# Optimization experiments

Measured on AMD Instinct MI355X. Metric: run time of the kernel, lower is better.

Reference implementation:

```python
import jax, jax.numpy as jnp
import numpy as np

B, S, D = 4, 2048, 1024
H, DK, DV = 16, 64, 64
FF = 4096
EPS = 1e-6


def _ln(x, g, b):
    mu = jnp.mean(x, axis=-1, keepdims=True)
    var = jnp.mean((x - mu) ** 2, axis=-1, keepdims=True)
    return (x - mu) * jax.lax.rsqrt(var + EPS) * g + b


def setup_inputs() -> dict:
    key = jax.random.key(0)
    ks = jax.random.split(key, 12)
    sd = 0.02
    return {
        "src": jax.random.normal(ks[0], (B, S, D), jnp.float32),
        "attn_mask": jnp.zeros((B, S, S), jnp.bool_),
        "Wq": jax.random.normal(ks[1], (D, H * DK), jnp.float32) * sd,
        "bq": jnp.zeros((H * DK,), jnp.float32),
        "Wk": jax.random.normal(ks[2], (D, H * DK), jnp.float32) * sd,
        "bk": jnp.zeros((H * DK,), jnp.float32),
        "Wv": jax.random.normal(ks[3], (D, H * DV), jnp.float32) * sd,
        "bv": jnp.zeros((H * DV,), jnp.float32),
        "Wo": jax.random.normal(ks[4], (D, D), jnp.float32) * sd,
        "bo": jnp.zeros((D,), jnp.float32),
        "ln1_g": jnp.ones((D,), jnp.float32),
        "ln1_b": jnp.zeros((D,), jnp.float32),
        "W1": jax.random.normal(ks[5], (D, FF), jnp.float32) * sd,
        "b1": jnp.zeros((FF,), jnp.float32),
        "W2": jax.random.normal(ks[6], (FF, D), jnp.float32) * sd,
        "b2": jnp.zeros((D,), jnp.float32),
        "ln2_g": jnp.ones((D,), jnp.float32),
        "ln2_b": jnp.zeros((D,), jnp.float32),
    }


def reference(src, attn_mask, Wq, bq, Wk, bk, Wv, bv, Wo, bo,
              ln1_g, ln1_b, W1, b1, W2, b2, ln2_g, ln2_b):
    # QKV projections, split heads: [B,S,H*dk] -> [B,H,S,dk]
    q = (src @ Wq + bq).reshape(B, S, H, DK).transpose(0, 2, 1, 3)
    k = (src @ Wk + bk).reshape(B, S, H, DK).transpose(0, 2, 1, 3)
    v = (src @ Wv + bv).reshape(B, S, H, DV).transpose(0, 2, 1, 3)

    scale = 1.0 / (DK ** 0.5)
    scores = jnp.einsum("bhqd,bhkd->bhqk", q, k) * scale
    scores = jnp.where(attn_mask[:, None, :, :], -1e9, scores)
    attn = jax.nn.softmax(scores, axis=-1)  # dropout = identity (eval)
    ctx = jnp.einsum("bhqk,bhkd->bhqd", attn, v)
    ctx = ctx.transpose(0, 2, 1, 3).reshape(B, S, D)

    att_out = ctx @ Wo + bo  # dropout = identity (eval)
    x = _ln(src + att_out, ln1_g, ln1_b)

    h = jax.nn.relu(x @ W1 + b1)  # dropout = identity (eval)
    ffn_out = h @ W2 + b2
    return _ln(ffn_out + x, ln2_g, ln2_b)
```

## Files before the change

### kernel.cpp

```cpp
#include <hip/hip_runtime.h>
#include <stdint.h>

#define BB 4
#define SS 2048
#define DMODEL 1024
#define NH 16
#define FF 4096
#define MROWS (BB*SS)

typedef __bf16 bf16x8 __attribute__((ext_vector_type(8)));
typedef __bf16 bf16x2t __attribute__((ext_vector_type(2)));
typedef float f32x4 __attribute__((ext_vector_type(4)));
typedef float f32x16 __attribute__((ext_vector_type(16)));
typedef unsigned uintx4 __attribute__((ext_vector_type(4)));

__device__ __forceinline__ unsigned short f2b(float f) {
  unsigned u = __float_as_uint(f);
  unsigned r = (u + 0x7FFFu + ((u >> 16) & 1u)) >> 16;
  return (unsigned short)r;
}

__device__ __forceinline__ unsigned pack2bf(float a, float b) {
  bf16x2t v = {(__bf16)a, (__bf16)b};
  return __builtin_bit_cast(unsigned, v);
}

__device__ __forceinline__ void pls32(unsigned& x, unsigned& y) {
#if defined(__has_builtin) && __has_builtin(__builtin_amdgcn_permlane32_swap)
  auto r = __builtin_amdgcn_permlane32_swap(x, y, 0, 0);
  x = (unsigned)r[0];
  y = (unsigned)r[1];
#else
  const unsigned sx = (unsigned)__shfl_xor((int)x, 32, 64);
  const unsigned sy = (unsigned)__shfl_xor((int)y, 32, 64);
  const bool hi = ((threadIdx.x >> 5) & 1) != 0;
  const unsigned nx = hi ? sy : x;
  const unsigned ny = hi ? y : sx;
  x = nx; y = ny;
#endif
}

__device__ __forceinline__ void gload_lds16(const void* g, void* l) {
  __builtin_amdgcn_global_load_lds(
      (const __attribute__((address_space(1))) void*)g,
      (__attribute__((address_space(3))) void*)l, 16, 0, 0);
}

__device__ __forceinline__ bf16x8 frag_rot(const unsigned short* base, int row, int kElem) {
  const int cb = kElem * 2;
  const unsigned off = (unsigned)(row * 128 + ((((cb >> 4) + row) & 7) << 4) + (cb & 15));
  return *reinterpret_cast<const bf16x8*>(reinterpret_cast<const char*>(base) + off);
}

__global__ __launch_bounds__(256) void f32_to_bf16_k(const float* __restrict__ in,
                                                     unsigned short* __restrict__ out, int n8) {
  const int i = blockIdx.x * 256 + threadIdx.x;
  if (i >= n8) return;
  const float4* p = reinterpret_cast<const float4*>(in) + (size_t)i * 2;
  const float4 a = p[0], c = p[1];
  uint4 o;
  o.x = (unsigned)f2b(a.x) | ((unsigned)f2b(a.y) << 16);
  o.y = (unsigned)f2b(a.z) | ((unsigned)f2b(a.w) << 16);
  o.z = (unsigned)f2b(c.x) | ((unsigned)f2b(c.y) << 16);
  o.w = (unsigned)f2b(c.z) | ((unsigned)f2b(c.w) << 16);
  reinterpret_cast<uint4*>(out)[i] = o;
}

__global__ __launch_bounds__(256) void transpose_convert_k(const float* __restrict__ in,
                                                           unsigned short* __restrict__ out,
                                                           int R, int C) {
  __shared__ float tile[32][33];
  const int c0 = blockIdx.x * 32, r0 = blockIdx.y * 32;
  const int tx = threadIdx.x, ty = threadIdx.y;
  #pragma unroll
  for (int i = 0; i < 4; ++i)
    tile[ty + i * 8][tx] = in[(size_t)(r0 + ty + i * 8) * C + c0 + tx];
  __syncthreads();
  #pragma unroll
  for (int i = 0; i < 4; ++i)
    out[(size_t)(c0 + ty + i * 8) * R + r0 + tx] = f2b(tile[tx][ty + i * 8]);
}

__global__ __launch_bounds__(256) void v_transpose_k(const unsigned short* __restrict__ Vb,
                                                     unsigned short* __restrict__ Vt) {
  __shared__ unsigned short tile[32][33];
  const int bh = blockIdx.z, b = bh >> 4, h = bh & 15;
  const int s0 = blockIdx.x * 32, d0 = blockIdx.y * 32;
  const int tx = threadIdx.x, ty = threadIdx.y;
  #pragma unroll
  for (int i = 0; i < 4; ++i)
    tile[ty + i * 8][tx] = Vb[(size_t)(b * SS + s0 + ty + i * 8) * DMODEL + h * 64 + d0 + tx];
  __syncthreads();
  #pragma unroll
  for (int i = 0; i < 4; ++i)
    Vt[(size_t)(bh * 64 + d0 + ty + i * 8) * SS + s0 + tx] = tile[tx][ty + i * 8];
}

__global__ __launch_bounds__(256) void mask_pack_k(const unsigned char* __restrict__ mask,
                                                   unsigned long long* __restrict__ mbits, int total) {
  const int idx = blockIdx.x * 256 + threadIdx.x;
  if (idx >= total) return;
  const uint4* p = reinterpret_cast<const uint4*>(mask) + (size_t)idx * 4;
  unsigned long long bits = 0ull;
  #pragma unroll
  for (int q = 0; q < 4; ++q) {
    uint4 v = p[q];
    unsigned wds[4] = {v.x, v.y, v.z, v.w};
    #pragma unroll
    for (int j = 0; j < 4; ++j)
      #pragma unroll
      for (int by = 0; by < 4; ++by)
        if ((wds[j] >> (by * 8)) & 0xFFu) bits |= 1ull << (q * 16 + j * 4 + by);
  }
  mbits[idx] = bits;
}

template <int EPI>
__global__ __launch_bounds__(256, 2) void gemm2_k(const unsigned short* __restrict__ A,
                                                  const unsigned short* __restrict__ Bt,
                                                  const float* __restrict__ bias_a,
                                                  const float* __restrict__ bias_b,
                                                  const float* __restrict__ bias_c,
                                                  void* __restrict__ Cout, int N, int K) {
  __shared__ __align__(16) unsigned short As[2][128 * 64];
  __shared__ __align__(16) unsigned short Bs[2][128 * 64];
  const int t = threadIdx.x;
  const int lane = t & 63, w = t >> 6;
  const int wr = w >> 1, wc = w & 1;
  const int lr = lane & 15, lg = lane >> 4;

  const int nwg = gridDim.x;
  const int q8 = nwg >> 3;
  const int wg = (blockIdx.x & 7) * q8 + (blockIdx.x >> 3);
  const int mb = wg & 63, nb = wg >> 6;
  const int m0 = mb * 128, n0 = nb * 128;

  const int srow = t >> 3;
  const int g = ((t & 7) - srow) & 7;
  const char* Asrc = reinterpret_cast<const char*>(A) + ((size_t)(m0 + srow) * K + g * 8) * 2;
  const char* Bsrc = reinterpret_cast<const char*>(Bt) + ((size_t)(n0 + srow) * K + g * 8) * 2;
  const size_t rstep = (size_t)32 * K * 2;
  char* AsB[2] = {reinterpret_cast<char*>(As[0]) + w * 1024, reinterpret_cast<char*>(As[1]) + w * 1024};
  char* BsB[2] = {reinterpret_cast<char*>(Bs[0]) + w * 1024, reinterpret_cast<char*>(Bs[1]) + w * 1024};

  auto stage = [&](int buf, int kt) {
    const char* ak = Asrc + (size_t)kt * 128;
    const char* bk = Bsrc + (size_t)kt * 128;
    #pragma unroll
    for (int c = 0; c < 4; ++c) {
      gload_lds16(ak + c * rstep, AsB[buf] + c * 4096);
      gload_lds16(bk + c * rstep, BsB[buf] + c * 4096);
    }
  };

  f32x4 acc[4][4] = {};
  const int nt = K >> 6;

  stage(0, 0);
  stage(1, 1);
  asm volatile("s_waitcnt vmcnt(8)" ::: "memory");
  __builtin_amdgcn_s_barrier();

  int cur = 0;
  for (int kt = 0; kt < nt; ++kt) {
    bf16x8 af[2][4], bfr[2][4];
    #pragma unroll
    for (int kk = 0; kk < 2; ++kk) {
      #pragma unroll
      for (int m = 0; m < 4; ++m)
        af[kk][m] = frag_rot(As[cur], wr * 64 + m * 16 + lr, kk * 32 + lg * 8);
      #pragma unroll
      for (int n = 0; n < 4; ++n)
        bfr[kk][n] = frag_rot(Bs[cur], wc * 64 + n * 16 + lr, kk * 32 + lg * 8);
    }
    __builtin_amdgcn_s_setprio(1);
    #pragma unroll
    for (int m = 0; m < 4; ++m)
      #pragma unroll
      for (int n = 0; n < 4; ++n)
        acc[m][n] = __builtin_amdgcn_mfma_f32_16x16x32_bf16(af[0][m], bfr[0][n], acc[m][n], 0, 0, 0);
    __builtin_amdgcn_s_setprio(0);

    asm volatile("s_waitcnt lgkmcnt(0)" ::: "memory");
    __builtin_amdgcn_s_barrier();
    if (kt + 2 < nt) {
      stage(cur, kt + 2);
      asm volatile("s_waitcnt vmcnt(8)" ::: "memory");
    } else {
      asm volatile("s_waitcnt vmcnt(0)" ::: "memory");
    }
    __builtin_amdgcn_s_barrier();
    __builtin_amdgcn_sched_barrier(0);

    __builtin_amdgcn_s_setprio(1);
    #pragma unroll
    for (int m = 0; m < 4; ++m)
      #pragma unroll
      for (int n = 0; n < 4; ++n)
        acc[m][n] = __builtin_amdgcn_mfma_f32_16x16x32_bf16(af[1][m], bfr[1][n], acc[m][n], 0, 0, 0);
    __builtin_amdgcn_s_setprio(0);
    cur ^= 1;
  }

  const int ccol0 = wc * 64;
  if constexpr (EPI == 3) {
    const int g3 = n0 >> 10;
    const float* bias = (g3 == 0) ? bias_a : (g3 == 1) ? bias_b : bias_c;
    unsigned short* Og = reinterpret_cast<unsigned short*>(Cout) + (size_t)g3 * MROWS * DMODEL;
    const int ncol0 = (n0 & 1023) + ccol0;
    float bv[4];
    #pragma unroll
    for (int n = 0; n < 4; ++n) bv[n] = bias[ncol0 + n * 16 + lr];
    #pragma unroll
    for (int m = 0; m < 4; ++m)
      #pragma unroll
      for (int n = 0; n < 4; ++n)
        #pragma unroll
        for (int i = 0; i < 4; ++i) {
          const float v = acc[m][n][i] + bv[n];
          const size_t row = (size_t)(m0 + wr * 64 + m * 16 + lg * 4 + i);
          Og[row * DMODEL + (ncol0 + n * 16 + lr)] = f2b(v);
        }
  } else {
    float bv[4];
    #pragma unroll
    for (int n = 0; n < 4; ++n) bv[n] = bias_a[n0 + ccol0 + n * 16 + lr];
    #pragma unroll
    for (int m = 0; m < 4; ++m)
      #pragma unroll
      for (int n = 0; n < 4; ++n)
        #pragma unroll
        for (int i = 0; i < 4; ++i) {
          float v = acc[m][n][i] + bv[n];
          if (EPI == 1) v = fmaxf(v, 0.0f);
          const size_t row = (size_t)(m0 + wr * 64 + m * 16 + lg * 4 + i);
          const size_t col = (size_t)(n0 + ccol0 + n * 16 + lr);
          if (EPI == 2) reinterpret_cast<float*>(Cout)[row * N + col] = v;
          else          reinterpret_cast<unsigned short*>(Cout)[row * N + col] = f2b(v);
        }
  }
}

__global__ __launch_bounds__(256) void attn4_k(const unsigned short* __restrict__ Qb,
                                               const unsigned short* __restrict__ Kb,
                                               const unsigned short* __restrict__ Vt,
                                               const unsigned long long* __restrict__ mbits,
                                               unsigned short* __restrict__ ctx) {
  __shared__ __align__(16) unsigned short smem[16384];
  unsigned short* KsC = smem;
  unsigned short* KsN = smem + 4096;
  unsigned short* VsC = smem + 8192;
  unsigned short* VsN = smem + 12288;

  const int t = threadIdx.x;
  const int lane = t & 63, w = t >> 6;
  const int lo = lane & 31, hi = lane >> 5;

  const int flat = blockIdx.x;
  const int bid = (flat & 7) * 128 + (flat >> 3);
  const int bh = bid >> 4, qb = bid & 15;
  const int b = bh >> 4, h = bh & 15;
  const int q0 = qb * 128 + w * 32;

  bf16x8 qf[4];
  {
    const unsigned short* qp = Qb + (size_t)(b * SS + q0 + lo) * DMODEL + h * 64 + hi * 8;
    #pragma unroll
    for (int ds = 0; ds < 4; ++ds) qf[ds] = *reinterpret_cast<const bf16x8*>(qp + ds * 16);
  }

  f32x16 ao0 = {}, ao1 = {};
  float lrun = 0.0f;
  const float C = 0.18033688011112042f;

  const int srow = t >> 3;
  const int gsw = ((t & 7) - srow) & 7;
  const char* Ksrc = reinterpret_cast<const char*>(Kb) +
                     ((size_t)(b * SS + srow) * DMODEL + h * 64 + gsw * 8) * 2;
  const char* Vsrc = reinterpret_cast<const char*>(Vt) +
                     ((size_t)(bh * 64 + srow) * SS + gsw * 8) * 2;
  const unsigned wdo = (unsigned)(w * 1024);

  auto stage = [&](int kv, unsigned short* Kbuf, unsigned short* Vbuf) {
    const char* ks0 = Ksrc + (size_t)kv * (64 * DMODEL * 2);
    const char* vs0 = Vsrc + (size_t)kv * 128;
    char* kd = reinterpret_cast<char*>(Kbuf) + wdo;
    char* vd = reinterpret_cast<char*>(Vbuf) + wdo;
    gload_lds16(ks0, kd);
    gload_lds16(ks0 + (size_t)32 * DMODEL * 2, kd + 4096);
    gload_lds16(vs0, vd);
    gload_lds16(vs0 + (size_t)32 * SS * 2, vd + 4096);
  };

  stage(0, KsC, VsC);
  asm volatile("s_waitcnt vmcnt(0)" ::: "memory");
  __syncthreads();

  for (int kv = 0; kv < SS / 64; ++kv) {
    if (kv + 1 < SS / 64) stage(kv + 1, KsN, VsN);

    const unsigned long long mb =
        mbits[(size_t)(b * SS + q0 + lo) * (SS / 64) + kv];

    f32x16 st0 = {}, st1 = {};
    __builtin_amdgcn_s_setprio(1);
    #pragma unroll
    for (int ds = 0; ds < 4; ++ds) {
      const int kcol = ds * 16 + hi * 8;
      const bf16x8 k0 = frag_rot(KsC, lo, kcol);
      const bf16x8 k1 = frag_rot(KsC, 32 + lo, kcol);
      st0 = __builtin_amdgcn_mfma_f32_32x32x16_bf16(k0, qf[ds], st0, 0, 0, 0);
      st1 = __builtin_amdgcn_mfma_f32_32x32x16_bf16(k1, qf[ds], st1, 0, 0, 0);
    }
    __builtin_amdgcn_s_setprio(0);

    if (__any(mb != 0ull)) {
      #pragma unroll
      for (int r = 0; r < 16; ++r) {
        const int k = (r & 3) + 8 * (r >> 2) + 4 * hi;
        if ((mb >> k) & 1ull) st0[r] = -8.0e9f;
        if ((mb >> (k + 32)) & 1ull) st1[r] = -8.0e9f;
      }
    }

    float ls = 0.0f;
    #pragma unroll
    for (int r = 0; r < 16; ++r) {
      st0[r] = exp2f(st0[r] * C);
      st1[r] = exp2f(st1[r] * C);
      ls += st0[r] + st1[r];
    }
    ls += __shfl_xor(ls, 32, 64);
    lrun += ls;

    unsigned pw[16];
    #define PACK8(SV, KB)                                            \
      {                                                              \
        unsigned c0 = pack2bf(SV[0], SV[1]);                         \
        unsigned c1 = pack2bf(SV[2], SV[3]);                         \
        unsigned c2 = pack2bf(SV[4], SV[5]);                         \
        unsigned c3 = pack2bf(SV[6], SV[7]);                         \
        unsigned c4 = pack2bf(SV[8], SV[9]);                         \
        unsigned c5 = pack2bf(SV[10], SV[11]);                       \
        unsigned c6 = pack2bf(SV[12], SV[13]);                       \
        unsigned c7 = pack2bf(SV[14], SV[15]);                       \
        pls32(c0, c2); pls32(c1, c3); pls32(c4, c6); pls32(c5, c7);  \
        pw[(KB) + 0] = c0; pw[(KB) + 1] = c1;                        \
        pw[(KB) + 2] = c2; pw[(KB) + 3] = c3;                        \
        pw[(KB) + 4] = c4; pw[(KB) + 5] = c5;                        \
        pw[(KB) + 6] = c6; pw[(KB) + 7] = c7;                        \
      }
    PACK8(st0, 0)
    PACK8(st1, 8)
    #undef PACK8

    __builtin_amdgcn_s_setprio(1);
    #pragma unroll
    for (int ks = 0; ks < 4; ++ks) {
      const uintx4 pv = {pw[ks * 4 + 0], pw[ks * 4 + 1], pw[ks * 4 + 2], pw[ks * 4 + 3]};
      const bf16x8 pb = __builtin_bit_cast(bf16x8, pv);
      const int scol = ks * 16 + hi * 8;
      ao0 = __builtin_amdgcn_mfma_f32_32x32x16_bf16(frag_rot(VsC, lo, scol), pb, ao0, 0, 0, 0);
      ao1 = __builtin_amdgcn_mfma_f32_32x32x16_bf16(frag_rot(VsC, 32 + lo, scol), pb, ao1, 0, 0, 0);
    }
    __builtin_amdgcn_s_setprio(0);

    asm volatile("s_waitcnt vmcnt(0)" ::: "memory");
    __syncthreads();
    unsigned short* tk = KsC; KsC = KsN; KsN = tk;
    unsigned short* tv = VsC; VsC = VsN; VsN = tv;
  }

  const float inv = 1.0f / lrun;
  unsigned short* Ob = smem + w * 2048;
  #pragma unroll
  for (int dt = 0; dt < 2; ++dt) {
    #pragma unroll
    for (int r = 0; r < 16; ++r) {
      const int d = dt * 32 + (r & 3) + 8 * (r >> 2) + 4 * hi;
      const float v = (dt ? ao1[r] : ao0[r]) * inv;
      const unsigned off = (unsigned)((lo * 128 + d * 2) ^ ((lo & 7) << 4));
      *reinterpret_cast<unsigned short*>(reinterpret_cast<char*>(Ob) + off) = f2b(v);
    }
  }
  __syncthreads();
  const int rr = lane >> 1, xh = (lane & 1) * 64;
  char* crow_g = reinterpret_cast<char*>(ctx) +
                 ((size_t)(b * SS + q0 + rr) * DMODEL + h * 64) * 2;
  #pragma unroll
  for (int c = 0; c < 4; ++c) {
    const unsigned off = (unsigned)((rr * 128 + xh + c * 16) ^ ((rr & 7) << 4));
    const uint4 vv = *reinterpret_cast<const uint4*>(reinterpret_cast<const char*>(Ob) + off);
    *reinterpret_cast<uint4*>(crow_g + xh + c * 16) = vv;
  }
}

__global__ __launch_bounds__(256) void ln_k(const float* __restrict__ a,
                                            const float* __restrict__ res,
                                            const float* __restrict__ g,
                                            const float* __restrict__ be,
                                            float* __restrict__ of,
                                            unsigned short* __restrict__ ob) {
  const int row = blockIdx.x, t = threadIdx.x;
  float4 v = reinterpret_cast<const float4*>(a + (size_t)row * DMODEL)[t];
  const float4 r = reinterpret_cast<const float4*>(res + (size_t)row * DMODEL)[t];
  v.x += r.x; v.y += r.y; v.z += r.z; v.w += r.w;
  float s = v.x + v.y + v.z + v.w;
  float ss = v.x * v.x + v.y * v.y + v.z * v.z + v.w * v.w;
  #pragma unroll
  for (int off = 1; off < 64; off <<= 1) {
    s += __shfl_xor(s, off, 64);
    ss += __shfl_xor(ss, off, 64);
  }
  __shared__ float red[8];
  const int wv = t >> 6;
  if ((t & 63) == 0) { red[wv] = s; red[4 + wv] = ss; }
  __syncthreads();
  s = red[0] + red[1] + red[2] + red[3];
  ss = red[4] + red[5] + red[6] + red[7];
  const float mu = s * (1.0f / DMODEL);
  const float rs = rsqrtf(ss * (1.0f / DMODEL) - mu * mu + 1e-6f);
  const float4 gg = reinterpret_cast<const float4*>(g)[t];
  const float4 bb = reinterpret_cast<const float4*>(be)[t];
  float4 o;
  o.x = (v.x - mu) * rs * gg.x + bb.x;
  o.y = (v.y - mu) * rs * gg.y + bb.y;
  o.z = (v.z - mu) * rs * gg.z + bb.z;
  o.w = (v.w - mu) * rs * gg.w + bb.w;
  if (of) reinterpret_cast<float4*>(of + (size_t)row * DMODEL)[t] = o;
  if (ob) {
    ushort4 u;
    u.x = f2b(o.x); u.y = f2b(o.y); u.z = f2b(o.z); u.w = f2b(o.w);
    reinterpret_cast<ushort4*>(ob + (size_t)row * DMODEL)[t] = u;
  }
}

extern "C" void kernel_launch(void* const* d_in, const int* in_sizes, int n_in,
                              void* d_out, int out_size, void* d_ws, size_t ws_size,
                              hipStream_t stream) {
  const float* src = (const float*)d_in[0];
  const unsigned char* mask = (const unsigned char*)d_in[1];
  const float* Wq = (const float*)d_in[2];
  const float* bq = (const float*)d_in[3];
  const float* Wk = (const float*)d_in[4];
  const float* bk = (const float*)d_in[5];
  const float* Wv = (const float*)d_in[6];
  const float* bv = (const float*)d_in[7];
  const float* Wo = (const float*)d_in[8];
  const float* bo = (const float*)d_in[9];
  const float* ln1_g = (const float*)d_in[10];
  const float* ln1_b = (const float*)d_in[11];
  const float* W1 = (const float*)d_in[12];
  const float* b1 = (const float*)d_in[13];
  const float* W2 = (const float*)d_in[14];
  const float* b2 = (const float*)d_in[15];
  const float* ln2_g = (const float*)d_in[16];
  const float* ln2_b = (const float*)d_in[17];

  char* ws = (char*)d_ws;
  size_t off = 0;
  auto alloc = [&](size_t bytes) {
    char* p = ws + off;
    off += (bytes + 255) & ~(size_t)255;
    return p;
  };
  unsigned short* srcb = (unsigned short*)alloc((size_t)MROWS * DMODEL * 2);
  unsigned short* WqT  = (unsigned short*)alloc((size_t)DMODEL * DMODEL * 2);
  unsigned short* WkT  = (unsigned short*)alloc((size_t)DMODEL * DMODEL * 2);
  unsigned short* WvT  = (unsigned short*)alloc((size_t)DMODEL * DMODEL * 2);
  unsigned short* WoT  = (unsigned short*)alloc((size_t)DMODEL * DMODEL * 2);
  unsigned short* W1T  = (unsigned short*)alloc((size_t)FF * DMODEL * 2);
  unsigned short* W2T  = (unsigned short*)alloc((size_t)DMODEL * FF * 2);
  unsigned short* Qb   = (unsigned short*)alloc((size_t)MROWS * DMODEL * 2);
  unsigned short* Kb   = (unsigned short*)alloc((size_t)MROWS * DMODEL * 2);
  unsigned short* Vb   = (unsigned short*)alloc((size_t)MROWS * DMODEL * 2);
  unsigned short* Vt   = (unsigned short*)alloc((size_t)MROWS * DMODEL * 2);
  unsigned short* ctx  = (unsigned short*)alloc((size_t)MROWS * DMODEL * 2);
  float*          xf   = (float*)alloc((size_t)MROWS * DMODEL * 4);
  unsigned short* xb   = (unsigned short*)alloc((size_t)MROWS * DMODEL * 2);
  unsigned short* hb   = (unsigned short*)alloc((size_t)MROWS * FF * 2);
  unsigned long long* mbits = (unsigned long long*)alloc((size_t)BB * SS * (SS / 64) * 8);
  float* outf = (float*)d_out;
  (void)Kb; (void)Vb;

  f32_to_bf16_k<<<(MROWS * DMODEL / 8 + 255) / 256, 256, 0, stream>>>(src, srcb, MROWS * DMODEL / 8);
  dim3 tb(32, 8);
  transpose_convert_k<<<dim3(32, 32), tb, 0, stream>>>(Wq, WqT, DMODEL, DMODEL);
  transpose_convert_k<<<dim3(32, 32), tb, 0, stream>>>(Wk, WkT, DMODEL, DMODEL);
  transpose_convert_k<<<dim3(32, 32), tb, 0, stream>>>(Wv, WvT, DMODEL, DMODEL);
  transpose_convert_k<<<dim3(32, 32), tb, 0, stream>>>(Wo, WoT, DMODEL, DMODEL);
  transpose_convert_k<<<dim3(FF / 32, 32), tb, 0, stream>>>(W1, W1T, DMODEL, FF);
  transpose_convert_k<<<dim3(32, FF / 32), tb, 0, stream>>>(W2, W2T, FF, DMODEL);
  mask_pack_k<<<(BB * SS * (SS / 64) + 255) / 256, 256, 0, stream>>>(mask, mbits, BB * SS * (SS / 64));

  gemm2_k<3><<<dim3(64 * 24), 256, 0, stream>>>(srcb, WqT, bq, bk, bv, Qb, 3072, DMODEL);

  v_transpose_k<<<dim3(SS / 32, 2, BB * NH), tb, 0, stream>>>(Vb, Vt);

  attn4_k<<<dim3((SS / 128) * BB * NH), 256, 0, stream>>>(Qb, Kb, Vt, mbits, ctx);

  gemm2_k<2><<<dim3(64 * 8), 256, 0, stream>>>(ctx, WoT, bo, nullptr, nullptr, outf, DMODEL, DMODEL);

  ln_k<<<MROWS, 256, 0, stream>>>(outf, src, ln1_g, ln1_b, xf, xb);

  gemm2_k<1><<<dim3(64 * 32), 256, 0, stream>>>(xb, W1T, b1, nullptr, nullptr, hb, FF, DMODEL);
  gemm2_k<2><<<dim3(64 * 8), 256, 0, stream>>>(hb, W2T, b2, nullptr, nullptr, outf, DMODEL, FF);

  ln_k<<<MROWS, 256, 0, stream>>>(outf, xf, ln2_g, ln2_b, outf, nullptr);
}
```

Before: 512.3 us.

## Replace GEMM with 256x256 eight-wave kernel, split-K output GEMMs, fold softmax scale

The 128x128, 4-wave GEMM is replaced by a 256x256, 8-wave kernel with XOR-swizzled LDS reads. Its k-step is split into four MFMA phases, with the A and B tile loads interleaved between them, to get more reuse per LDS byte and better overlap of loads with compute. The two N=1024 GEMMs (Wo and W2) now use split-K by two. Their partial sums go to two fp32 buffers, and the second buffer is added inside the LayerNorm kernel, so that enough blocks are launched. The softmax log2 scale is folded into the Q projection epilogue, the masked-score value changes to a small finite constant, and the row-sum reduction becomes a tree. This adds an extra fp32 read in LayerNorm, reuses the Q buffer as scratch, and the finite mask value gives masked keys a tiny nonzero weight.

```diff
diff --git a/kernel.cpp b/kernel.cpp
--- a/kernel.cpp
+++ b/kernel.cpp
@@ -115,129 +115,179 @@
   mbits[idx] = bits;
 }
 
+#define CQ 0.18033688011112042f
 template <int EPI>
-__global__ __launch_bounds__(256, 2) void gemm2_k(const unsigned short* __restrict__ A,
-                                                  const unsigned short* __restrict__ Bt,
-                                                  const float* __restrict__ bias_a,
-                                                  const float* __restrict__ bias_b,
-                                                  const float* __restrict__ bias_c,
-                                                  void* __restrict__ Cout, int N, int K) {
-  __shared__ __align__(16) unsigned short As[2][128 * 64];
-  __shared__ __align__(16) unsigned short Bs[2][128 * 64];
-  const int t = threadIdx.x;
-  const int lane = t & 63, w = t >> 6;
-  const int wr = w >> 1, wc = w & 1;
+__global__ __launch_bounds__(512, 2) void gemm3_k(
+    const unsigned short* __restrict__ A, int lda,
+    const unsigned short* __restrict__ Bt, int ldb,
+    const float* __restrict__ ba, const float* __restrict__ bb,
+    const float* __restrict__ bc,
+    float* __restrict__ C0, float* __restrict__ C1,
+    unsigned short* __restrict__ Cb,
+    int N, int K, int gn) {
+  __shared__ __align__(16) unsigned short As[2][256 * 64];
+  __shared__ __align__(16) unsigned short Bs[2][256 * 64];
+
+  const int t = threadIdx.x, lane = t & 63, w = t >> 6;
+  const int wr = w >> 2, wc = w & 3;
   const int lr = lane & 15, lg = lane >> 4;
 
   const int nwg = gridDim.x;
   const int q8 = nwg >> 3;
-  const int wg = (blockIdx.x & 7) * q8 + (blockIdx.x >> 3);
-  const int mb = wg & 63, nb = wg >> 6;
-  const int m0 = mb * 128, n0 = nb * 128;
-
-  const int srow = t >> 3;
-  const int g = ((t & 7) - srow) & 7;
-  const char* Asrc = reinterpret_cast<const char*>(A) + ((size_t)(m0 + srow) * K + g * 8) * 2;
-  const char* Bsrc = reinterpret_cast<const char*>(Bt) + ((size_t)(n0 + srow) * K + g * 8) * 2;
-  const size_t rstep = (size_t)32 * K * 2;
-  char* AsB[2] = {reinterpret_cast<char*>(As[0]) + w * 1024, reinterpret_cast<char*>(As[1]) + w * 1024};
-  char* BsB[2] = {reinterpret_cast<char*>(Bs[0]) + w * 1024, reinterpret_cast<char*>(Bs[1]) + w * 1024};
-
-  auto stage = [&](int buf, int kt) {
-    const char* ak = Asrc + (size_t)kt * 128;
-    const char* bk = Bsrc + (size_t)kt * 128;
-    #pragma unroll
-    for (int c = 0; c < 4; ++c) {
-      gload_lds16(ak + c * rstep, AsB[buf] + c * 4096);
-      gload_lds16(bk + c * rstep, BsB[buf] + c * 4096);
-    }
+  int wg = ((int)blockIdx.x & 7) * q8 + ((int)blockIdx.x >> 3);
+  const int per = 32 * gn;
+  const int sp = wg / per;
+  wg -= sp * per;
+  const int nb = wg >> 5, mb = wg & 31;
+  const int m0 = mb * 256, n0 = nb * 256;
+  const size_t k0 = (size_t)sp * K;
+
+  const int srow8 = lane >> 3;
+  const int glog = (lane & 7) ^ (srow8 & 7);
+  const int arow = w * 8 + srow8;
+  const unsigned short* Abase = A + (size_t)(m0 + arow) * lda + k0 + glog * 8;
+  const unsigned short* Bbase = Bt + (size_t)(n0 + arow) * ldb + k0 + glog * 8;
+
+  auto stageA = [&](int slot, int kt) {
+    #pragma unroll
+    for (int j = 0; j < 4; ++j)
+      gload_lds16(Abase + (size_t)j * 64 * lda + kt * 64,
+                  reinterpret_cast<char*>(&As[slot][0]) + w * 1024 + j * 8192);
   };
-
-  f32x4 acc[4][4] = {};
+  auto stageB = [&](int slot, int kt) {
+    #pragma unroll
+    for (int j = 0; j < 4; ++j)
+      gload_lds16(Bbase + (size_t)j * 64 * ldb + kt * 64,
+                  reinterpret_cast<char*>(&Bs[slot][0]) + w * 1024 + j * 8192);
+  };
+  auto rdA = [&](int slot, int mf, int kk) -> bf16x8 {
+    const int row = wr * 128 + mf * 16 + lr;
+    const unsigned off = (unsigned)(row * 128 + (((unsigned)(kk * 64 + lg * 16)) ^ ((unsigned)(lr & 7) << 4)));
+    return *reinterpret_cast<const bf16x8*>(reinterpret_cast<const char*>(&As[slot][0]) + off);
+  };
+  auto rdB = [&](int slot, int nf, int kk) -> bf16x8 {
+    const int row = wc * 64 + nf * 16 + lr;
+    const unsigned off = (unsigned)(row * 128 + (((unsigned)(kk * 64 + lg * 16)) ^ ((unsigned)(lr & 7) << 4)));
+    return *reinterpret_cast<const bf16x8*>(reinterpret_cast<const char*>(&Bs[slot][0]) + off);
+  };
+
+  f32x4 acc[8][4] = {};
   const int nt = K >> 6;
 
-  stage(0, 0);
-  stage(1, 1);
+  stageA(0, 0); stageB(0, 0);
+  if (nt > 1) { stageA(1, 1); stageB(1, 1); }
   asm volatile("s_waitcnt vmcnt(8)" ::: "memory");
   __builtin_amdgcn_s_barrier();
 
-  int cur = 0;
   for (int kt = 0; kt < nt; ++kt) {
-    bf16x8 af[2][4], bfr[2][4];
-    #pragma unroll
-    for (int kk = 0; kk < 2; ++kk) {
-      #pragma unroll
-      for (int m = 0; m < 4; ++m)
-        af[kk][m] = frag_rot(As[cur], wr * 64 + m * 16 + lr, kk * 32 + lg * 8);
-      #pragma unroll
-      for (int n = 0; n < 4; ++n)
-        bfr[kk][n] = frag_rot(Bs[cur], wc * 64 + n * 16 + lr, kk * 32 + lg * 8);
-    }
+    const int s = kt & 1;
+    bf16x8 a0[8], b0[4], a1[8], b1[4];
+
+    #pragma unroll
+    for (int m = 0; m < 8; ++m) a0[m] = rdA(s, m, 0);
+    #pragma unroll
+    for (int n = 0; n < 4; ++n) b0[n] = rdB(s, n, 0);
+    __builtin_amdgcn_s_barrier();
+    asm volatile("s_waitcnt lgkmcnt(0)" ::: "memory");
+    __builtin_amdgcn_sched_barrier(0);
     __builtin_amdgcn_s_setprio(1);
     #pragma unroll
-    for (int m = 0; m < 4; ++m)
-      #pragma unroll
-      for (int n = 0; n < 4; ++n)
-        acc[m][n] = __builtin_amdgcn_mfma_f32_16x16x32_bf16(af[0][m], bfr[0][n], acc[m][n], 0, 0, 0);
+    for (int m = 0; m < 8; ++m)
+      #pragma unroll
+      for (int n = 0; n < 2; ++n)
+        acc[m][n] = __builtin_amdgcn_mfma_f32_16x16x32_bf16(a0[m], b0[n], acc[m][n], 0, 0, 0);
     __builtin_amdgcn_s_setprio(0);
-
+    __builtin_amdgcn_s_barrier();
+
+    #pragma unroll
+    for (int m = 0; m < 8; ++m) a1[m] = rdA(s, m, 1);
+    #pragma unroll
+    for (int n = 0; n < 4; ++n) b1[n] = rdB(s, n, 1);
+    __builtin_amdgcn_s_barrier();
+    __builtin_amdgcn_s_setprio(1);
+    #pragma unroll
+    for (int m = 0; m < 8; ++m)
+      #pragma unroll
+      for (int n = 2; n < 4; ++n)
+        acc[m][n] = __builtin_amdgcn_mfma_f32_16x16x32_bf16(a0[m], b0[n], acc[m][n], 0, 0, 0);
+    __builtin_amdgcn_s_setprio(0);
     asm volatile("s_waitcnt lgkmcnt(0)" ::: "memory");
     __builtin_amdgcn_s_barrier();
+
+    if (kt + 2 < nt) stageA(s, kt + 2);
+    __builtin_amdgcn_s_barrier();
+    __builtin_amdgcn_s_setprio(1);
+    #pragma unroll
+    for (int m = 0; m < 8; ++m)
+      #pragma unroll
+      for (int n = 0; n < 2; ++n)
+        acc[m][n] = __builtin_amdgcn_mfma_f32_16x16x32_bf16(a1[m], b1[n], acc[m][n], 0, 0, 0);
+    __builtin_amdgcn_s_setprio(0);
+    __builtin_amdgcn_s_barrier();
+
     if (kt + 2 < nt) {
-      stage(cur, kt + 2);
+      stageB(s, kt + 2);
       asm volatile("s_waitcnt vmcnt(8)" ::: "memory");
     } else {
       asm volatile("s_waitcnt vmcnt(0)" ::: "memory");
     }
     __builtin_amdgcn_s_barrier();
-    __builtin_amdgcn_sched_barrier(0);
-
     __builtin_amdgcn_s_setprio(1);
     #pragma unroll
-    for (int m = 0; m < 4; ++m)
-      #pragma unroll
-      for (int n = 0; n < 4; ++n)
-        acc[m][n] = __builtin_amdgcn_mfma_f32_16x16x32_bf16(af[1][m], bfr[1][n], acc[m][n], 0, 0, 0);
+    for (int m = 0; m < 8; ++m)
+      #pragma unroll
+      for (int n = 2; n < 4; ++n)
+        acc[m][n] = __builtin_amdgcn_mfma_f32_16x16x32_bf16(a1[m], b1[n], acc[m][n], 0, 0, 0);
     __builtin_amdgcn_s_setprio(0);
-    cur ^= 1;
-  }
-
-  const int ccol0 = wc * 64;
+    __builtin_amdgcn_s_barrier();
+  }
+
   if constexpr (EPI == 3) {
     const int g3 = n0 >> 10;
-    const float* bias = (g3 == 0) ? bias_a : (g3 == 1) ? bias_b : bias_c;
-    unsigned short* Og = reinterpret_cast<unsigned short*>(Cout) + (size_t)g3 * MROWS * DMODEL;
-    const int ncol0 = (n0 & 1023) + ccol0;
-    float bv[4];
-    #pragma unroll
-    for (int n = 0; n < 4; ++n) bv[n] = bias[ncol0 + n * 16 + lr];
-    #pragma unroll
-    for (int m = 0; m < 4; ++m)
-      #pragma unroll
-      for (int n = 0; n < 4; ++n)
+    const float* bias = (g3 == 0) ? ba : (g3 == 1) ? bb : bc;
+    unsigned short* Og = Cb + (size_t)g3 * MROWS * DMODEL;
+    const float scl = (g3 == 0) ? CQ : 1.0f;
+    #pragma unroll
+    for (int n = 0; n < 4; ++n) {
+      const int col = (n0 & 1023) + wc * 64 + n * 16 + lr;
+      const float bv = bias[col];
+      #pragma unroll
+      for (int m = 0; m < 8; ++m)
         #pragma unroll
         for (int i = 0; i < 4; ++i) {
-          const float v = acc[m][n][i] + bv[n];
-          const size_t row = (size_t)(m0 + wr * 64 + m * 16 + lg * 4 + i);
-          Og[row * DMODEL + (ncol0 + n * 16 + lr)] = f2b(v);
+          const float v = (acc[m][n][i] + bv) * scl;
+          const size_t row = (size_t)(m0 + wr * 128 + m * 16 + lg * 4 + i);
+          Og[row * DMODEL + col] = f2b(v);
         }
-  } else {
-    float bv[4];
-    #pragma unroll
-    for (int n = 0; n < 4; ++n) bv[n] = bias_a[n0 + ccol0 + n * 16 + lr];
-    #pragma unroll
-    for (int m = 0; m < 4; ++m)
-      #pragma unroll
-      for (int n = 0; n < 4; ++n)
+    }
+  } else if constexpr (EPI == 1) {
+    #pragma unroll
+    for (int n = 0; n < 4; ++n) {
+      const int col = n0 + wc * 64 + n * 16 + lr;
+      const float bv = ba[col];
+      #pragma unroll
+      for (int m = 0; m < 8; ++m)
         #pragma unroll
         for (int i = 0; i < 4; ++i) {
-          float v = acc[m][n][i] + bv[n];
-          if (EPI == 1) v = fmaxf(v, 0.0f);
-          const size_t row = (size_t)(m0 + wr * 64 + m * 16 + lg * 4 + i);
-          const size_t col = (size_t)(n0 + ccol0 + n * 16 + lr);
-          if (EPI == 2) reinterpret_cast<float*>(Cout)[row * N + col] = v;
-          else          reinterpret_cast<unsigned short*>(Cout)[row * N + col] = f2b(v);
+          const float v = fmaxf(acc[m][n][i] + bv, 0.0f);
+          const size_t row = (size_t)(m0 + wr * 128 + m * 16 + lg * 4 + i);
+          Cb[row * N + col] = f2b(v);
         }
+    }
+  } else {
+    float* Of = (sp == 0) ? C0 : C1;
+    #pragma unroll
+    for (int n = 0; n < 4; ++n) {
+      const int col = n0 + wc * 64 + n * 16 + lr;
+      const float bv = (sp == 0) ? ba[col] : 0.0f;
+      #pragma unroll
+      for (int m = 0; m < 8; ++m)
+        #pragma unroll
+        for (int i = 0; i < 4; ++i) {
+          const size_t row = (size_t)(m0 + wr * 128 + m * 16 + lg * 4 + i);
+          Of[row * N + col] = acc[m][n][i] + bv;
+        }
+    }
   }
 }
 
@@ -271,7 +321,6 @@
 
   f32x16 ao0 = {}, ao1 = {};
   float lrun = 0.0f;
-  const float C = 0.18033688011112042f;
 
   const int srow = t >> 3;
   const int gsw = ((t & 7) - srow) & 7;
@@ -318,18 +367,23 @@
       #pragma unroll
       for (int r = 0; r < 16; ++r) {
         const int k = (r & 3) + 8 * (r >> 2) + 4 * hi;
-        if ((mb >> k) & 1ull) st0[r] = -8.0e9f;
-        if ((mb >> (k + 32)) & 1ull) st1[r] = -8.0e9f;
+        if ((mb >> k) & 1ull) st0[r] = -20.0f;
+        if ((mb >> (k + 32)) & 1ull) st1[r] = -20.0f;
       }
     }
 
-    float ls = 0.0f;
+    float ps[16];
     #pragma unroll
     for (int r = 0; r < 16; ++r) {
-      st0[r] = exp2f(st0[r] * C);
-      st1[r] = exp2f(st1[r] * C);
-      ls += st0[r] + st1[r];
-    }
+      st0[r] = exp2f(st0[r]);
+      st1[r] = exp2f(st1[r]);
+      ps[r] = st0[r] + st1[r];
+    }
+    #pragma unroll
+    for (int r = 0; r < 8; ++r) ps[r] += ps[r + 8];
+    #pragma unroll
+    for (int r = 0; r < 4; ++r) ps[r] += ps[r + 4];
+    float ls = (ps[0] + ps[1]) + (ps[2] + ps[3]);
     ls += __shfl_xor(ls, 32, 64);
     lrun += ls;
 
@@ -396,6 +450,7 @@
 }
 
 __global__ __launch_bounds__(256) void ln_k(const float* __restrict__ a,
+                                            const float* __restrict__ a2,
                                             const float* __restrict__ res,
                                             const float* __restrict__ g,
                                             const float* __restrict__ be,
@@ -405,6 +460,10 @@
   float4 v = reinterpret_cast<const float4*>(a + (size_t)row * DMODEL)[t];
   const float4 r = reinterpret_cast<const float4*>(res + (size_t)row * DMODEL)[t];
   v.x += r.x; v.y += r.y; v.z += r.z; v.w += r.w;
+  if (a2) {
+    const float4 p = reinterpret_cast<const float4*>(a2 + (size_t)row * DMODEL)[t];
+    v.x += p.x; v.y += p.y; v.z += p.z; v.w += p.w;
+  }
   float s = v.x + v.y + v.z + v.w;
   float ss = v.x * v.x + v.y * v.y + v.z * v.z + v.w * v.w;
   #pragma unroll
@@ -480,6 +539,7 @@
   unsigned short* xb   = (unsigned short*)alloc((size_t)MROWS * DMODEL * 2);
   unsigned short* hb   = (unsigned short*)alloc((size_t)MROWS * FF * 2);
   unsigned long long* mbits = (unsigned long long*)alloc((size_t)BB * SS * (SS / 64) * 8);
+  float* p2 = reinterpret_cast<float*>(Qb);
   float* outf = (float*)d_out;
   (void)Kb; (void)Vb;
 
@@ -493,18 +553,26 @@
   transpose_convert_k<<<dim3(32, FF / 32), tb, 0, stream>>>(W2, W2T, FF, DMODEL);
   mask_pack_k<<<(BB * SS * (SS / 64) + 255) / 256, 256, 0, stream>>>(mask, mbits, BB * SS * (SS / 64));
 
-  gemm2_k<3><<<dim3(64 * 24), 256, 0, stream>>>(srcb, WqT, bq, bk, bv, Qb, 3072, DMODEL);
+  gemm3_k<3><<<dim3(384), 512, 0, stream>>>(srcb, DMODEL, WqT, DMODEL,
+                                            bq, bk, bv, nullptr, nullptr, Qb,
+                                            3072, DMODEL, 12);
 
   v_transpose_k<<<dim3(SS / 32, 2, BB * NH), tb, 0, stream>>>(Vb, Vt);
 
   attn4_k<<<dim3((SS / 128) * BB * NH), 256, 0, stream>>>(Qb, Kb, Vt, mbits, ctx);
 
-  gemm2_k<2><<<dim3(64 * 8), 256, 0, stream>>>(ctx, WoT, bo, nullptr, nullptr, outf, DMODEL, DMODEL);
-
-  ln_k<<<MROWS, 256, 0, stream>>>(outf, src, ln1_g, ln1_b, xf, xb);
-
-  gemm2_k<1><<<dim3(64 * 32), 256, 0, stream>>>(xb, W1T, b1, nullptr, nullptr, hb, FF, DMODEL);
-  gemm2_k<2><<<dim3(64 * 8), 256, 0, stream>>>(hb, W2T, b2, nullptr, nullptr, outf, DMODEL, FF);
-
-  ln_k<<<MROWS, 256, 0, stream>>>(outf, xf, ln2_g, ln2_b, outf, nullptr);
-}
+  gemm3_k<4><<<dim3(256), 512, 0, stream>>>(ctx, DMODEL, WoT, DMODEL,
+                                            bo, nullptr, nullptr, outf, p2, nullptr,
+                                            DMODEL, DMODEL / 2, 4);
+
+  ln_k<<<MROWS, 256, 0, stream>>>(outf, p2, src, ln1_g, ln1_b, xf, xb);
+
+  gemm3_k<1><<<dim3(512), 512, 0, stream>>>(xb, DMODEL, W1T, DMODEL,
+                                            b1, nullptr, nullptr, nullptr, nullptr, hb,
+                                            FF, DMODEL, 16);
+  gemm3_k<4><<<dim3(256), 512, 0, stream>>>(hb, FF, W2T, FF,
+                                            b2, nullptr, nullptr, outf, p2, nullptr,
+                                            DMODEL, FF / 2, 4);
+
+  ln_k<<<MROWS, 256, 0, stream>>>(outf, p2, xf, ln2_g, ln2_b, outf, nullptr);
+}
```

Result: slower. 557.4 us (+8.8%).

## Load K/V fragments directly from global in attention, fold softmax scale into Q

Applied to the files above, without the earlier changes.

The attention kernel no longer stages K and V tiles through double-buffered LDS with barriers. Each wave now reads its MFMA fragments straight from global memory, relying on cache reuse. The softmax scale (log2e/sqrt(dk)) is folded into the Q projection epilogue, so the inner loop does a bare exp2. The masked value becomes -20 in the scaled domain, which treats exp2(-20) as effectively zero. The GEMM LDS swizzle changes from rotation to XOR. Possible costs are more global traffic and latency from uncoalesced fragment loads, and a masked fill that is not exactly zero. The removed final __syncthreads is only safe because each wave writes and reads its own LDS slice.

```diff
diff --git a/kernel.cpp b/kernel.cpp
--- a/kernel.cpp
+++ b/kernel.cpp
@@ -46,9 +46,8 @@
       (__attribute__((address_space(3))) void*)l, 16, 0, 0);
 }
 
-__device__ __forceinline__ bf16x8 frag_rot(const unsigned short* base, int row, int kElem) {
-  const int cb = kElem * 2;
-  const unsigned off = (unsigned)(row * 128 + ((((cb >> 4) + row) & 7) << 4) + (cb & 15));
+__device__ __forceinline__ bf16x8 lds_frag(const unsigned short* base, int row, int k) {
+  unsigned off = (unsigned)((row * 128 + k * 2) ^ ((row & 7) << 4));
   return *reinterpret_cast<const bf16x8*>(reinterpret_cast<const char*>(base) + off);
 }
 
@@ -115,6 +114,7 @@
   mbits[idx] = bits;
 }
 
+#define CQ 0.18033688011112042f
 template <int EPI>
 __global__ __launch_bounds__(256, 2) void gemm2_k(const unsigned short* __restrict__ A,
                                                   const unsigned short* __restrict__ Bt,
@@ -136,9 +136,9 @@
   const int m0 = mb * 128, n0 = nb * 128;
 
   const int srow = t >> 3;
-  const int g = ((t & 7) - srow) & 7;
-  const char* Asrc = reinterpret_cast<const char*>(A) + ((size_t)(m0 + srow) * K + g * 8) * 2;
-  const char* Bsrc = reinterpret_cast<const char*>(Bt) + ((size_t)(n0 + srow) * K + g * 8) * 2;
+  const unsigned cxor = (unsigned)(((t & 7) * 16) ^ (((t >> 3) & 7) << 4));
+  const char* Asrc = reinterpret_cast<const char*>(A) + ((size_t)(m0 + srow) * K) * 2 + cxor;
+  const char* Bsrc = reinterpret_cast<const char*>(Bt) + ((size_t)(n0 + srow) * K) * 2 + cxor;
   const size_t rstep = (size_t)32 * K * 2;
   char* AsB[2] = {reinterpret_cast<char*>(As[0]) + w * 1024, reinterpret_cast<char*>(As[1]) + w * 1024};
   char* BsB[2] = {reinterpret_cast<char*>(Bs[0]) + w * 1024, reinterpret_cast<char*>(Bs[1]) + w * 1024};
@@ -168,10 +168,10 @@
     for (int kk = 0; kk < 2; ++kk) {
       #pragma unroll
       for (int m = 0; m < 4; ++m)
-        af[kk][m] = frag_rot(As[cur], wr * 64 + m * 16 + lr, kk * 32 + lg * 8);
+        af[kk][m] = lds_frag(As[cur], wr * 64 + m * 16 + lr, kk * 32 + lg * 8);
       #pragma unroll
       for (int n = 0; n < 4; ++n)
-        bfr[kk][n] = frag_rot(Bs[cur], wc * 64 + n * 16 + lr, kk * 32 + lg * 8);
+        bfr[kk][n] = lds_frag(Bs[cur], wc * 64 + n * 16 + lr, kk * 32 + lg * 8);
     }
     __builtin_amdgcn_s_setprio(1);
     #pragma unroll
@@ -206,6 +206,7 @@
   if constexpr (EPI == 3) {
     const int g3 = n0 >> 10;
     const float* bias = (g3 == 0) ? bias_a : (g3 == 1) ? bias_b : bias_c;
+    const float scl = (g3 == 0) ? CQ : 1.0f;
     unsigned short* Og = reinterpret_cast<unsigned short*>(Cout) + (size_t)g3 * MROWS * DMODEL;
     const int ncol0 = (n0 & 1023) + ccol0;
     float bv[4];
@@ -217,7 +218,7 @@
       for (int n = 0; n < 4; ++n)
         #pragma unroll
         for (int i = 0; i < 4; ++i) {
-          const float v = acc[m][n][i] + bv[n];
+          const float v = (acc[m][n][i] + bv[n]) * scl;
           const size_t row = (size_t)(m0 + wr * 64 + m * 16 + lg * 4 + i);
           Og[row * DMODEL + (ncol0 + n * 16 + lr)] = f2b(v);
         }
@@ -241,16 +242,12 @@
   }
 }
 
-__global__ __launch_bounds__(256) void attn4_k(const unsigned short* __restrict__ Qb,
+__global__ __launch_bounds__(256) void attn5_k(const unsigned short* __restrict__ Qb,
                                                const unsigned short* __restrict__ Kb,
                                                const unsigned short* __restrict__ Vt,
                                                const unsigned long long* __restrict__ mbits,
                                                unsigned short* __restrict__ ctx) {
-  __shared__ __align__(16) unsigned short smem[16384];
-  unsigned short* KsC = smem;
-  unsigned short* KsN = smem + 4096;
-  unsigned short* VsC = smem + 8192;
-  unsigned short* VsN = smem + 12288;
+  __shared__ __align__(16) unsigned short Obs[4][2048];
 
   const int t = threadIdx.x;
   const int lane = t & 63, w = t >> 6;
@@ -269,67 +266,49 @@
     for (int ds = 0; ds < 4; ++ds) qf[ds] = *reinterpret_cast<const bf16x8*>(qp + ds * 16);
   }
 
+  const unsigned short* Kh = Kb + (size_t)b * SS * DMODEL + h * 64;
+  const unsigned short* Vh = Vt + (size_t)bh * 64 * SS;
+  const unsigned long long* mrow = mbits + (size_t)(b * SS + q0 + lo) * (SS / 64);
+
   f32x16 ao0 = {}, ao1 = {};
   float lrun = 0.0f;
-  const float C = 0.18033688011112042f;
-
-  const int srow = t >> 3;
-  const int gsw = ((t & 7) - srow) & 7;
-  const char* Ksrc = reinterpret_cast<const char*>(Kb) +
-                     ((size_t)(b * SS + srow) * DMODEL + h * 64 + gsw * 8) * 2;
-  const char* Vsrc = reinterpret_cast<const char*>(Vt) +
-                     ((size_t)(bh * 64 + srow) * SS + gsw * 8) * 2;
-  const unsigned wdo = (unsigned)(w * 1024);
-
-  auto stage = [&](int kv, unsigned short* Kbuf, unsigned short* Vbuf) {
-    const char* ks0 = Ksrc + (size_t)kv * (64 * DMODEL * 2);
-    const char* vs0 = Vsrc + (size_t)kv * 128;
-    char* kd = reinterpret_cast<char*>(Kbuf) + wdo;
-    char* vd = reinterpret_cast<char*>(Vbuf) + wdo;
-    gload_lds16(ks0, kd);
-    gload_lds16(ks0 + (size_t)32 * DMODEL * 2, kd + 4096);
-    gload_lds16(vs0, vd);
-    gload_lds16(vs0 + (size_t)32 * SS * 2, vd + 4096);
-  };
-
-  stage(0, KsC, VsC);
-  asm volatile("s_waitcnt vmcnt(0)" ::: "memory");
-  __syncthreads();
 
   for (int kv = 0; kv < SS / 64; ++kv) {
-    if (kv + 1 < SS / 64) stage(kv + 1, KsN, VsN);
-
-    const unsigned long long mb =
-        mbits[(size_t)(b * SS + q0 + lo) * (SS / 64) + kv];
-
+    const int kv0 = kv * 64;
+    const unsigned long long mb = mrow[kv];
+
+    const unsigned short* kp0 = Kh + (size_t)(kv0 + lo) * DMODEL + hi * 8;
+    const unsigned short* kp1 = kp0 + (size_t)32 * DMODEL;
     f32x16 st0 = {}, st1 = {};
-    __builtin_amdgcn_s_setprio(1);
     #pragma unroll
     for (int ds = 0; ds < 4; ++ds) {
-      const int kcol = ds * 16 + hi * 8;
-      const bf16x8 k0 = frag_rot(KsC, lo, kcol);
-      const bf16x8 k1 = frag_rot(KsC, 32 + lo, kcol);
+      const bf16x8 k0 = *reinterpret_cast<const bf16x8*>(kp0 + ds * 16);
+      const bf16x8 k1 = *reinterpret_cast<const bf16x8*>(kp1 + ds * 16);
       st0 = __builtin_amdgcn_mfma_f32_32x32x16_bf16(k0, qf[ds], st0, 0, 0, 0);
       st1 = __builtin_amdgcn_mfma_f32_32x32x16_bf16(k1, qf[ds], st1, 0, 0, 0);
     }
-    __builtin_amdgcn_s_setprio(0);
 
     if (__any(mb != 0ull)) {
       #pragma unroll
       for (int r = 0; r < 16; ++r) {
         const int k = (r & 3) + 8 * (r >> 2) + 4 * hi;
-        if ((mb >> k) & 1ull) st0[r] = -8.0e9f;
-        if ((mb >> (k + 32)) & 1ull) st1[r] = -8.0e9f;
+        if ((mb >> k) & 1ull) st0[r] = -20.0f;
+        if ((mb >> (k + 32)) & 1ull) st1[r] = -20.0f;
       }
     }
 
-    float ls = 0.0f;
+    float ps[16];
     #pragma unroll
     for (int r = 0; r < 16; ++r) {
-      st0[r] = exp2f(st0[r] * C);
-      st1[r] = exp2f(st1[r] * C);
-      ls += st0[r] + st1[r];
-    }
+      st0[r] = exp2f(st0[r]);
+      st1[r] = exp2f(st1[r]);
+      ps[r] = st0[r] + st1[r];
+    }
+    #pragma unroll
+    for (int r = 0; r < 8; ++r) ps[r] += ps[r + 8];
+    #pragma unroll
+    for (int r = 0; r < 4; ++r) ps[r] += ps[r + 4];
+    float ls = (ps[0] + ps[1]) + (ps[2] + ps[3]);
     ls += __shfl_xor(ls, 32, 64);
     lrun += ls;
 
@@ -354,25 +333,21 @@
     PACK8(st1, 8)
     #undef PACK8
 
-    __builtin_amdgcn_s_setprio(1);
+    const unsigned short* vp0 = Vh + (size_t)lo * SS + kv0 + hi * 8;
+    const unsigned short* vp1 = vp0 + (size_t)32 * SS;
     #pragma unroll
     for (int ks = 0; ks < 4; ++ks) {
       const uintx4 pv = {pw[ks * 4 + 0], pw[ks * 4 + 1], pw[ks * 4 + 2], pw[ks * 4 + 3]};
       const bf16x8 pb = __builtin_bit_cast(bf16x8, pv);
-      const int scol = ks * 16 + hi * 8;
-      ao0 = __builtin_amdgcn_mfma_f32_32x32x16_bf16(frag_rot(VsC, lo, scol), pb, ao0, 0, 0, 0);
-      ao1 = __builtin_amdgcn_mfma_f32_32x32x16_bf16(frag_rot(VsC, 32 + lo, scol), pb, ao1, 0, 0, 0);
-    }
-    __builtin_amdgcn_s_setprio(0);
-
-    asm volatile("s_waitcnt vmcnt(0)" ::: "memory");
-    __syncthreads();
-    unsigned short* tk = KsC; KsC = KsN; KsN = tk;
-    unsigned short* tv = VsC; VsC = VsN; VsN = tv;
+      const bf16x8 v0 = *reinterpret_cast<const bf16x8*>(vp0 + ks * 16);
+      const bf16x8 v1 = *reinterpret_cast<const bf16x8*>(vp1 + ks * 16);
+      ao0 = __builtin_amdgcn_mfma_f32_32x32x16_bf16(v0, pb, ao0, 0, 0, 0);
+      ao1 = __builtin_amdgcn_mfma_f32_32x32x16_bf16(v1, pb, ao1, 0, 0, 0);
+    }
   }
 
   const float inv = 1.0f / lrun;
-  unsigned short* Ob = smem + w * 2048;
+  unsigned short* Ob = &Obs[w][0];
   #pragma unroll
   for (int dt = 0; dt < 2; ++dt) {
     #pragma unroll
@@ -383,7 +358,6 @@
       *reinterpret_cast<unsigned short*>(reinterpret_cast<char*>(Ob) + off) = f2b(v);
     }
   }
-  __syncthreads();
   const int rr = lane >> 1, xh = (lane & 1) * 64;
   char* crow_g = reinterpret_cast<char*>(ctx) +
                  ((size_t)(b * SS + q0 + rr) * DMODEL + h * 64) * 2;
@@ -497,7 +471,7 @@
 
   v_transpose_k<<<dim3(SS / 32, 2, BB * NH), tb, 0, stream>>>(Vb, Vt);
 
-  attn4_k<<<dim3((SS / 128) * BB * NH), 256, 0, stream>>>(Qb, Kb, Vt, mbits, ctx);
+  attn5_k<<<dim3((SS / 128) * BB * NH), 256, 0, stream>>>(Qb, Kb, Vt, mbits, ctx);
 
   gemm2_k<2><<<dim3(64 * 8), 256, 0, stream>>>(ctx, WoT, bo, nullptr, nullptr, outf, DMODEL, DMODEL);
 
```

Measured after the change: 612.4 us. 1.2x slower.
